# Kernel tuning notes

Hardware: AMD Instinct MI355X
Metric: run time of the kernel (lower is better)

The kernel has to match this reference:

```python
import jax, jax.numpy as jnp
import numpy as np

N_NODES = 100_000
N_EDGES = 1_600_000
IN_DIM = 500
HID = 128
OUT = 16
DEG = 3          # Chebyshev 'order' -> DEG+1 basis terms
N_KAN_USED = 2   # forward applies kan_layers[:num_layers-1] with num_layers=3


def spmm(edge_index, h):
    # torch.sparse.mm(A, h) with A = COO(edge_index, ones, (N, N)):
    # out[row] = sum over edges of h[col]
    return jax.ops.segment_sum(h[edge_index[1]], edge_index[0], num_segments=N_NODES)


def cheb_kan(h, coeffs):
    # ChebyKANLayer: t = tanh(h); basis T_k(t) = cos(k*arccos(t)) computed via
    # the (mathematically identical, numerically stable) recurrence.
    t = jnp.tanh(h)                                  # [N, HID]
    Ts = [jnp.ones_like(t), t]
    for _ in range(DEG - 1):
        Ts.append(2.0 * t * Ts[-1] - Ts[-2])
    basis = jnp.stack(Ts, axis=-1)                   # [N, HID, DEG+1]
    return jnp.einsum('nid,iod->no', basis, coeffs)  # [N, HID]


def setup_inputs() -> dict:
    key = jax.random.key(0)
    ks = jax.random.split(key, 6)
    x = jax.random.normal(ks[0], (N_NODES, IN_DIM), dtype=jnp.float32)
    edge_index = jax.random.randint(ks[1], (2, N_EDGES), 0, N_NODES)
    W_in = jax.random.normal(ks[2], (IN_DIM, HID), dtype=jnp.float32) / np.sqrt(IN_DIM)
    cheb_coeffs = jax.random.normal(ks[3], (N_KAN_USED, HID, HID, DEG + 1),
                                    dtype=jnp.float32) / (HID * (DEG + 1))
    W_out = jax.random.normal(ks[4], (HID, OUT), dtype=jnp.float32) / np.sqrt(HID)
    return {"x": x, "edge_index": edge_index, "W_in": W_in,
            "cheb_coeffs": cheb_coeffs, "W_out": W_out}


def reference(x, edge_index, W_in, cheb_coeffs, W_out):
    h = x @ W_in                      # linear_input (no bias)
    # dropout is identity at inference
    h = spmm(edge_index, h)           # sparse adjacency aggregation
    for l in range(N_KAN_USED):
        h = cheb_kan(h, cheb_coeffs[l])
        h = spmm(edge_index, h)
    logits = h @ W_out                # output_layer (no bias)
    return jax.nn.log_softmax(logits, axis=-1)
```

## Files before the change

kernel.cpp:

```cpp
#include <hip/hip_runtime.h>
#include <hip/hip_bf16.h>

#define N_NODES 100000
#define N_EDGES 1600000
#define IN_DIM  500
#define HID     128
#define KDIM    512
#define NB      782
#define BCAP    4096

typedef __attribute__((ext_vector_type(8))) short bf16x8;
typedef __attribute__((ext_vector_type(4))) float f32x4;

__device__ inline short f2bf(float x) {
    union { float f; unsigned u; } v; v.f = x;
    unsigned r = (v.u + 0x7FFFu + ((v.u >> 16) & 1u)) >> 16;
    return (short)r;
}
__device__ inline float bf_lo(unsigned u) { union { unsigned u; float f; } v; v.u = u << 16; return v.f; }
__device__ inline float bf_hi(unsigned u) { union { unsigned u; float f; } v; v.u = u & 0xFFFF0000u; return v.f; }
__device__ inline float bf2f(unsigned short s) { union { unsigned u; float f; } v; v.u = ((unsigned)s) << 16; return v.f; }


__global__ __launch_bounds__(256) void bin_kernel(const int* __restrict__ ei,
                                                  int* __restrict__ bcnt,
                                                  unsigned* __restrict__ buf) {
    int e = blockIdx.x * 256 + threadIdx.x;
    if (e < N_EDGES) {
        int r = ei[e];
        int c = ei[N_EDGES + e];
        int b = r >> 7;
        int p = atomicAdd(&bcnt[b * 16], 1);
        if (p < BCAP) buf[b * BCAP + p] = ((unsigned)(r & 127) << 17) | (unsigned)c;
    }
}

__global__ __launch_bounds__(1024) void bscan_kernel(const int* __restrict__ bcnt,
                                                     int* __restrict__ bbase) {
    __shared__ int buf[1024];
    const int tid = threadIdx.x;
    int v = (tid < NB) ? bcnt[tid * 16] : 0;
    buf[tid] = v;
    __syncthreads();
    for (int off = 1; off < 1024; off <<= 1) {
        int t = (tid >= off) ? buf[tid - off] : 0;
        __syncthreads();
        buf[tid] += t;
        __syncthreads();
    }
    if (tid < NB) bbase[tid] = buf[tid] - v;
}

__global__ __launch_bounds__(256) void place_kernel(const unsigned* __restrict__ buf,
                                                    const int* __restrict__ bcnt,
                                                    const int* __restrict__ bbase,
                                                    int* __restrict__ row_start,
                                                    int* __restrict__ col_sorted) {
    __shared__ int hist[128];
    __shared__ int scan[128];
    __shared__ int cur[128];
    const int b = blockIdx.x, tid = threadIdx.x;
    int cnt = bcnt[b * 16]; if (cnt > BCAP) cnt = BCAP;
    const int base = bbase[b];
    if (tid < 128) hist[tid] = 0;
    __syncthreads();
    for (int i = tid; i < cnt; i += 256)
        atomicAdd(&hist[buf[b * BCAP + i] >> 17], 1);
    __syncthreads();
    if (tid < 128) scan[tid] = hist[tid];
    __syncthreads();
    for (int off = 1; off < 128; off <<= 1) {
        int t = (tid < 128 && tid >= off) ? scan[tid - off] : 0;
        __syncthreads();
        if (tid < 128) scan[tid] += t;
        __syncthreads();
    }
    if (tid < 128) {
        int excl = scan[tid] - hist[tid] + base;
        cur[tid] = excl;
        int r = b * 128 + tid;
        if (r < N_NODES) row_start[r] = excl;
        if (r == N_NODES - 1) row_start[N_NODES] = excl + hist[tid];
    }
    __syncthreads();
    for (int i = tid; i < cnt; i += 256) {
        unsigned u = buf[b * BCAP + i];
        int rl = (int)(u >> 17);
        int c  = (int)(u & 0x1FFFFu);
        int pos = atomicAdd(&cur[rl], 1);
        col_sorted[pos] = c;
    }
}

__global__ __launch_bounds__(256) void repack_cheb(const float* __restrict__ cheb,
                                                   unsigned short* __restrict__ Bmat) {
    int idx = blockIdx.x * 256 + threadIdx.x;
    int l = idx >> 16;
    int rem = idx & 65535;
    int o = rem >> 9;
    int k = rem & 511;
    int i = k >> 2;
    int d = k & 3;
    Bmat[idx] = (unsigned short)f2bf(cheb[l * 65536 + i * 512 + o * 4 + d]);
}
__global__ __launch_bounds__(256) void repack_w(const float* __restrict__ W,
                                                unsigned short* __restrict__ Wmat) {
    int idx = blockIdx.x * 256 + threadIdx.x;
    int o = idx >> 9;
    int k = idx & 511;
    Wmat[idx] = (k < IN_DIM) ? (unsigned short)f2bf(W[k * HID + o]) : 0;
}

__global__ __launch_bounds__(256, 3) void gemm_xw(const float* __restrict__ x,
                                                  const unsigned short* __restrict__ Wmat,
                                                  unsigned short* __restrict__ out) {
    __shared__ __align__(16) short As[128][40];
    __shared__ __align__(16) short Bs[128][40];
    const int tid  = threadIdx.x;
    const int lane = tid & 63;
    const int wave = tid >> 6;
    const int quad = lane >> 4;
    const int l16  = lane & 15;
    const int n0   = blockIdx.x * 128;
    const int lr   = tid >> 1;
    const int lh   = tid & 1;

    f32x4 acc[2][8];
#pragma unroll
    for (int mt = 0; mt < 2; mt++)
#pragma unroll
        for (int nt = 0; nt < 8; nt++)
#pragma unroll
            for (int r = 0; r < 4; r++) acc[mt][nt][r] = 0.f;

    for (int kt = 0; kt < 16; kt++) {
        const int k0 = kt * 32;
        {
            int n = n0 + lr; if (n >= N_NODES) n = N_NODES - 1;
            const float* src = x + (long)n * IN_DIM + k0 + lh * 16;
            const int kb = k0 + lh * 16;
            float v[16];
            if (kb + 16 <= IN_DIM) {
                const float4* s4 = (const float4*)src;
                float4 a0 = s4[0], a1 = s4[1], a2 = s4[2], a3 = s4[3];
                v[0]=a0.x; v[1]=a0.y; v[2]=a0.z; v[3]=a0.w;
                v[4]=a1.x; v[5]=a1.y; v[6]=a1.z; v[7]=a1.w;
                v[8]=a2.x; v[9]=a2.y; v[10]=a2.z; v[11]=a2.w;
                v[12]=a3.x; v[13]=a3.y; v[14]=a3.z; v[15]=a3.w;
            } else {
#pragma unroll
                for (int q = 0; q < 16; q++) v[q] = (kb + q < IN_DIM) ? src[q] : 0.f;
            }
            short tmp[16];
#pragma unroll
            for (int q = 0; q < 16; q++) tmp[q] = f2bf(v[q]);
            *(bf16x8*)&As[lr][lh * 16]     = *(bf16x8*)&tmp[0];
            *(bf16x8*)&As[lr][lh * 16 + 8] = *(bf16x8*)&tmp[8];
        }
        for (int idx = tid; idx < 512; idx += 256) {
            int m = idx >> 2, kq = idx & 3;
            *(bf16x8*)&Bs[m][kq * 8] = *(const bf16x8*)&Wmat[m * 512 + k0 + kq * 8];
        }
        __syncthreads();
        bf16x8 a0 = *(const bf16x8*)&As[wave * 32 + l16][quad * 8];
        bf16x8 a1 = *(const bf16x8*)&As[wave * 32 + 16 + l16][quad * 8];
#pragma unroll
        for (int nt = 0; nt < 8; nt++) {
            bf16x8 b = *(const bf16x8*)&Bs[nt * 16 + l16][quad * 8];
            acc[0][nt] = __builtin_amdgcn_mfma_f32_16x16x32_bf16(a0, b, acc[0][nt], 0, 0, 0);
            acc[1][nt] = __builtin_amdgcn_mfma_f32_16x16x32_bf16(a1, b, acc[1][nt], 0, 0, 0);
        }
        __syncthreads();
    }
#pragma unroll
    for (int mt = 0; mt < 2; mt++) {
        int mrow = n0 + wave * 32 + mt * 16 + quad * 4;
#pragma unroll
        for (int r = 0; r < 4; r++) {
            int n = mrow + r;
            if (n < N_NODES) {
#pragma unroll
                for (int nt = 0; nt < 8; nt++)
                    out[(long)n * HID + nt * 16 + l16] = (unsigned short)f2bf(acc[mt][nt][r]);
            }
        }
    }
}

__global__ __launch_bounds__(256, 3) void cheb_gemm(const unsigned short* __restrict__ h,
                                                    const unsigned short* __restrict__ Bmat,
                                                    unsigned short* __restrict__ out) {
    __shared__ __align__(16) short As[128][40];
    __shared__ __align__(16) short Bs[128][40];
    const int tid  = threadIdx.x;
    const int lane = tid & 63;
    const int wave = tid >> 6;
    const int quad = lane >> 4;
    const int l16  = lane & 15;
    const int n0   = blockIdx.x * 128;
    const int lr   = tid >> 1;
    const int lh   = tid & 1;

    f32x4 acc[2][8];
#pragma unroll
    for (int mt = 0; mt < 2; mt++)
#pragma unroll
        for (int nt = 0; nt < 8; nt++)
#pragma unroll
            for (int r = 0; r < 4; r++) acc[mt][nt][r] = 0.f;

    for (int kt = 0; kt < 16; kt++) {
        const int k0 = kt * 32;
        const int i0 = kt * 8;
        {
            int n = n0 + lr; if (n >= N_NODES) n = N_NODES - 1;
            const ushort4 hv = *(const ushort4*)(h + (long)n * HID + i0 + lh * 4);
            float hx[4] = {bf2f(hv.x), bf2f(hv.y), bf2f(hv.z), bf2f(hv.w)};
            short tmp[16];
#pragma unroll
            for (int q = 0; q < 4; q++) {
                float xx = fminf(fmaxf(hx[q], -15.f), 15.f);
                float e  = __expf(2.f * xx);
                float t  = (e - 1.f) / (e + 1.f);
                float T2 = 2.f * t * t - 1.f;
                float T3 = 2.f * t * T2 - t;
                tmp[q * 4 + 0] = (short)0x3F80;
                tmp[q * 4 + 1] = f2bf(t);
                tmp[q * 4 + 2] = f2bf(T2);
                tmp[q * 4 + 3] = f2bf(T3);
            }
            *(bf16x8*)&As[lr][lh * 16]     = *(bf16x8*)&tmp[0];
            *(bf16x8*)&As[lr][lh * 16 + 8] = *(bf16x8*)&tmp[8];
        }
        for (int idx = tid; idx < 512; idx += 256) {
            int m = idx >> 2, kq = idx & 3;
            *(bf16x8*)&Bs[m][kq * 8] = *(const bf16x8*)&Bmat[m * 512 + k0 + kq * 8];
        }
        __syncthreads();
        bf16x8 a0 = *(const bf16x8*)&As[wave * 32 + l16][quad * 8];
        bf16x8 a1 = *(const bf16x8*)&As[wave * 32 + 16 + l16][quad * 8];
#pragma unroll
        for (int nt = 0; nt < 8; nt++) {
            bf16x8 b = *(const bf16x8*)&Bs[nt * 16 + l16][quad * 8];
            acc[0][nt] = __builtin_amdgcn_mfma_f32_16x16x32_bf16(a0, b, acc[0][nt], 0, 0, 0);
            acc[1][nt] = __builtin_amdgcn_mfma_f32_16x16x32_bf16(a1, b, acc[1][nt], 0, 0, 0);
        }
        __syncthreads();
    }
#pragma unroll
    for (int mt = 0; mt < 2; mt++) {
        int mrow = n0 + wave * 32 + mt * 16 + quad * 4;
#pragma unroll
        for (int r = 0; r < 4; r++) {
            int n = mrow + r;
            if (n < N_NODES) {
#pragma unroll
                for (int nt = 0; nt < 8; nt++)
                    out[(long)n * HID + nt * 16 + l16] = (unsigned short)f2bf(acc[mt][nt][r]);
            }
        }
    }
}

__global__ __launch_bounds__(256) void spmm_gather(const int* __restrict__ row_start,
                                                   const int* __restrict__ col_sorted,
                                                   const unsigned short* __restrict__ h,
                                                   unsigned short* __restrict__ out) {
    const int wid  = (blockIdx.x * 256 + threadIdx.x) >> 6;
    const int lane = threadIdx.x & 63;
    if (wid >= N_NODES) return;
    const int s = row_start[wid];
    const int e = row_start[wid + 1];
    const unsigned* __restrict__ h1 = (const unsigned*)h;
    float ax0 = 0.f, ay0 = 0.f, ax1 = 0.f, ay1 = 0.f;
    float ax2 = 0.f, ay2 = 0.f, ax3 = 0.f, ay3 = 0.f;
    int j = s;
    for (; j + 3 < e; j += 4) {
        int c0 = col_sorted[j];
        int c1 = col_sorted[j + 1];
        int c2 = col_sorted[j + 2];
        int c3 = col_sorted[j + 3];
        unsigned u0 = h1[c0 * 64 + lane];
        unsigned u1 = h1[c1 * 64 + lane];
        unsigned u2 = h1[c2 * 64 + lane];
        unsigned u3 = h1[c3 * 64 + lane];
        ax0 += bf_lo(u0); ay0 += bf_hi(u0);
        ax1 += bf_lo(u1); ay1 += bf_hi(u1);
        ax2 += bf_lo(u2); ay2 += bf_hi(u2);
        ax3 += bf_lo(u3); ay3 += bf_hi(u3);
    }
    for (; j < e; j++) {
        unsigned u = h1[col_sorted[j] * 64 + lane];
        ax0 += bf_lo(u); ay0 += bf_hi(u);
    }
    ax0 += ax1 + ax2 + ax3; ay0 += ay1 + ay2 + ay3;
    unsigned lo = (unsigned)(unsigned short)f2bf(ax0);
    unsigned hi = (unsigned)(unsigned short)f2bf(ay0);
    ((unsigned*)out)[wid * 64 + lane] = lo | (hi << 16);
}

__global__ __launch_bounds__(256) void out_kernel(const unsigned short* __restrict__ h,
                                                  const float* __restrict__ Wo,
                                                  float* __restrict__ out) {
    __shared__ float Ws[HID * 16];
    __shared__ float Hs[16][HID];
    const int tid = threadIdx.x;
    const int n0 = blockIdx.x * 16;
    for (int idx = tid; idx < HID * 16; idx += 256) Ws[idx] = Wo[idx];
    const unsigned* h1 = (const unsigned*)h;
    for (int idx = tid; idx < 16 * 64; idx += 256) {
        int nl = idx >> 6;
        int kp = idx & 63;
        unsigned u = h1[(n0 + nl) * 64 + kp];
        Hs[nl][kp * 2]     = bf_lo(u);
        Hs[nl][kp * 2 + 1] = bf_hi(u);
    }
    __syncthreads();
    const int nl = tid >> 4;
    const int o  = tid & 15;
    float acc = 0.f;
#pragma unroll
    for (int k = 0; k < HID; k++) acc += Hs[nl][k] * Ws[k * 16 + o];
    float mx = acc;
#pragma unroll
    for (int m = 8; m >= 1; m >>= 1) mx = fmaxf(mx, __shfl_xor(mx, m));
    float ex = expf(acc - mx);
    float se = ex;
#pragma unroll
    for (int m = 8; m >= 1; m >>= 1) se += __shfl_xor(se, m);
    out[(n0 + nl) * 16 + o] = acc - mx - logf(se);
}


extern "C" void kernel_launch(void* const* d_in, const int* in_sizes, int n_in,
                              void* d_out, int out_size, void* d_ws, size_t ws_size,
                              hipStream_t stream) {
    const float* x     = (const float*)d_in[0];
    const int*   ei    = (const int*)d_in[1];
    const float* W_in  = (const float*)d_in[2];
    const float* cheb  = (const float*)d_in[3];
    const float* W_out = (const float*)d_in[4];
    float* out = (float*)d_out;

    char* p = (char*)d_ws;
    unsigned short* hA   = (unsigned short*)p; p += (size_t)N_NODES * HID * 2;
    unsigned short* hB   = (unsigned short*)p; p += (size_t)N_NODES * HID * 2;
    int*   col_sorted    = (int*)p;            p += (size_t)N_EDGES * 4;
    unsigned short* Bmat = (unsigned short*)p; p += (size_t)2 * HID * KDIM * 2;
    unsigned short* Wmat = (unsigned short*)p; p += (size_t)HID * KDIM * 2;
    int*   row_start     = (int*)p;            p += (size_t)(N_NODES + 1) * 4;
    int*   bcnt          = (int*)p;            p += (size_t)NB * 16 * 4;
    int*   bbase         = (int*)p;            p += (size_t)NB * 4;

    unsigned* bbuf = (unsigned*)hA;

    const int nblk_gemm = (N_NODES + 127) / 128;
    const int nblk_edge = N_EDGES / 256;
    const int nblk_spmm = (N_NODES + 3) / 4;
    const int nblk_out  = N_NODES / 16;

    hipMemsetAsync(bcnt, 0, (size_t)NB * 16 * 4, stream);
    bin_kernel<<<nblk_edge, 256, 0, stream>>>(ei, bcnt, bbuf);
    bscan_kernel<<<1, 1024, 0, stream>>>(bcnt, bbase);
    place_kernel<<<NB, 256, 0, stream>>>(bbuf, bcnt, bbase, row_start, col_sorted);
    repack_cheb<<<2 * HID * KDIM / 256, 256, 0, stream>>>(cheb, Bmat);
    repack_w<<<HID * KDIM / 256, 256, 0, stream>>>(W_in, Wmat);

    gemm_xw<<<nblk_gemm, 256, 0, stream>>>(x, Wmat, hA);
    spmm_gather<<<nblk_spmm, 256, 0, stream>>>(row_start, col_sorted, hA, hB);

    cheb_gemm<<<nblk_gemm, 256, 0, stream>>>(hB, Bmat, hA);
    spmm_gather<<<nblk_spmm, 256, 0, stream>>>(row_start, col_sorted, hA, hB);

    cheb_gemm<<<nblk_gemm, 256, 0, stream>>>(hB, Bmat + HID * KDIM, hA);
    spmm_gather<<<nblk_spmm, 256, 0, stream>>>(row_start, col_sorted, hA, hB);

    out_kernel<<<nblk_out, 256, 0, stream>>>(hB, W_out, out);
}
```

Baseline: 740.9 us.

## Load GEMM operands directly into MFMA registers, dropping LDS staging and barriers

Both the input projection GEMM and the Chebyshev GEMM stop staging A and B tiles through shared memory. Each lane now loads its MFMA fragment straight from global memory (x rows, h rows, and the weight matrix through cache) and computes the tanh/Chebyshev basis per lane. This removes the LDS round trips and the two __syncthreads per k-step, and the k-loop is unrolled by two. In exchange, every wave re-reads the weight fragments from L1/L2, the x loads become 32-byte strided accesses per lane, and launch bounds are relaxed to allow more registers per thread.

```diff
diff --git a/kernel.cpp b/kernel.cpp
--- a/kernel.cpp
+++ b/kernel.cpp
@@ -111,19 +111,20 @@
     Wmat[idx] = (k < IN_DIM) ? (unsigned short)f2bf(W[k * HID + o]) : 0;
 }
 
-__global__ __launch_bounds__(256, 3) void gemm_xw(const float* __restrict__ x,
+__global__ __launch_bounds__(256, 2) void gemm_xw(const float* __restrict__ x,
                                                   const unsigned short* __restrict__ Wmat,
                                                   unsigned short* __restrict__ out) {
-    __shared__ __align__(16) short As[128][40];
-    __shared__ __align__(16) short Bs[128][40];
     const int tid  = threadIdx.x;
     const int lane = tid & 63;
     const int wave = tid >> 6;
     const int quad = lane >> 4;
     const int l16  = lane & 15;
     const int n0   = blockIdx.x * 128;
-    const int lr   = tid >> 1;
-    const int lh   = tid & 1;
+
+    int row0 = n0 + wave * 32 + l16;      if (row0 >= N_NODES) row0 = N_NODES - 1;
+    int row1 = n0 + wave * 32 + 16 + l16; if (row1 >= N_NODES) row1 = N_NODES - 1;
+    const float* __restrict__ xr0 = x + (long)row0 * IN_DIM + quad * 8;
+    const float* __restrict__ xr1 = x + (long)row1 * IN_DIM + quad * 8;
 
     f32x4 acc[2][8];
 #pragma unroll
@@ -133,44 +134,43 @@
 #pragma unroll
             for (int r = 0; r < 4; r++) acc[mt][nt][r] = 0.f;
 
-    for (int kt = 0; kt < 16; kt++) {
+#pragma unroll 2
+    for (int kt = 0; kt < 15; kt++) {
         const int k0 = kt * 32;
-        {
-            int n = n0 + lr; if (n >= N_NODES) n = N_NODES - 1;
-            const float* src = x + (long)n * IN_DIM + k0 + lh * 16;
-            const int kb = k0 + lh * 16;
-            float v[16];
-            if (kb + 16 <= IN_DIM) {
-                const float4* s4 = (const float4*)src;
-                float4 a0 = s4[0], a1 = s4[1], a2 = s4[2], a3 = s4[3];
-                v[0]=a0.x; v[1]=a0.y; v[2]=a0.z; v[3]=a0.w;
-                v[4]=a1.x; v[5]=a1.y; v[6]=a1.z; v[7]=a1.w;
-                v[8]=a2.x; v[9]=a2.y; v[10]=a2.z; v[11]=a2.w;
-                v[12]=a3.x; v[13]=a3.y; v[14]=a3.z; v[15]=a3.w;
-            } else {
-#pragma unroll
-                for (int q = 0; q < 16; q++) v[q] = (kb + q < IN_DIM) ? src[q] : 0.f;
-            }
-            short tmp[16];
-#pragma unroll
-            for (int q = 0; q < 16; q++) tmp[q] = f2bf(v[q]);
-            *(bf16x8*)&As[lr][lh * 16]     = *(bf16x8*)&tmp[0];
-            *(bf16x8*)&As[lr][lh * 16 + 8] = *(bf16x8*)&tmp[8];
-        }
-        for (int idx = tid; idx < 512; idx += 256) {
-            int m = idx >> 2, kq = idx & 3;
-            *(bf16x8*)&Bs[m][kq * 8] = *(const bf16x8*)&Wmat[m * 512 + k0 + kq * 8];
-        }
-        __syncthreads();
-        bf16x8 a0 = *(const bf16x8*)&As[wave * 32 + l16][quad * 8];
-        bf16x8 a1 = *(const bf16x8*)&As[wave * 32 + 16 + l16][quad * 8];
+        float4 f0a = *(const float4*)(xr0 + k0);
+        float4 f0b = *(const float4*)(xr0 + k0 + 4);
+        float4 f1a = *(const float4*)(xr1 + k0);
+        float4 f1b = *(const float4*)(xr1 + k0 + 4);
+        short t0[8] = {f2bf(f0a.x), f2bf(f0a.y), f2bf(f0a.z), f2bf(f0a.w),
+                       f2bf(f0b.x), f2bf(f0b.y), f2bf(f0b.z), f2bf(f0b.w)};
+        short t1[8] = {f2bf(f1a.x), f2bf(f1a.y), f2bf(f1a.z), f2bf(f1a.w),
+                       f2bf(f1b.x), f2bf(f1b.y), f2bf(f1b.z), f2bf(f1b.w)};
+        bf16x8 a0 = *(bf16x8*)t0;
+        bf16x8 a1 = *(bf16x8*)t1;
 #pragma unroll
         for (int nt = 0; nt < 8; nt++) {
-            bf16x8 b = *(const bf16x8*)&Bs[nt * 16 + l16][quad * 8];
+            bf16x8 b = *(const bf16x8*)&Wmat[(nt * 16 + l16) * 512 + k0 + quad * 8];
             acc[0][nt] = __builtin_amdgcn_mfma_f32_16x16x32_bf16(a0, b, acc[0][nt], 0, 0, 0);
             acc[1][nt] = __builtin_amdgcn_mfma_f32_16x16x32_bf16(a1, b, acc[1][nt], 0, 0, 0);
         }
-        __syncthreads();
+    }
+    {
+        const int k0 = 480;
+        short t0[8], t1[8];
+#pragma unroll
+        for (int q = 0; q < 8; q++) {
+            int kk = k0 + quad * 8 + q;
+            t0[q] = (kk < IN_DIM) ? f2bf(xr0[k0 + q]) : (short)0;
+            t1[q] = (kk < IN_DIM) ? f2bf(xr1[k0 + q]) : (short)0;
+        }
+        bf16x8 a0 = *(bf16x8*)t0;
+        bf16x8 a1 = *(bf16x8*)t1;
+#pragma unroll
+        for (int nt = 0; nt < 8; nt++) {
+            bf16x8 b = *(const bf16x8*)&Wmat[(nt * 16 + l16) * 512 + k0 + quad * 8];
+            acc[0][nt] = __builtin_amdgcn_mfma_f32_16x16x32_bf16(a0, b, acc[0][nt], 0, 0, 0);
+            acc[1][nt] = __builtin_amdgcn_mfma_f32_16x16x32_bf16(a1, b, acc[1][nt], 0, 0, 0);
+        }
     }
 #pragma unroll
     for (int mt = 0; mt < 2; mt++) {
@@ -187,19 +187,20 @@
     }
 }
 
-__global__ __launch_bounds__(256, 3) void cheb_gemm(const unsigned short* __restrict__ h,
+__global__ __launch_bounds__(256, 2) void cheb_gemm(const unsigned short* __restrict__ h,
                                                     const unsigned short* __restrict__ Bmat,
                                                     unsigned short* __restrict__ out) {
-    __shared__ __align__(16) short As[128][40];
-    __shared__ __align__(16) short Bs[128][40];
     const int tid  = threadIdx.x;
     const int lane = tid & 63;
     const int wave = tid >> 6;
     const int quad = lane >> 4;
     const int l16  = lane & 15;
     const int n0   = blockIdx.x * 128;
-    const int lr   = tid >> 1;
-    const int lh   = tid & 1;
+
+    int row0 = n0 + wave * 32 + l16;      if (row0 >= N_NODES) row0 = N_NODES - 1;
+    int row1 = n0 + wave * 32 + 16 + l16; if (row1 >= N_NODES) row1 = N_NODES - 1;
+    const unsigned* __restrict__ hr0 = (const unsigned*)(h + (long)row0 * HID) + quad;
+    const unsigned* __restrict__ hr1 = (const unsigned*)(h + (long)row1 * HID) + quad;
 
     f32x4 acc[2][8];
 #pragma unroll
@@ -209,43 +210,50 @@
 #pragma unroll
             for (int r = 0; r < 4; r++) acc[mt][nt][r] = 0.f;
 
+#pragma unroll 2
     for (int kt = 0; kt < 16; kt++) {
         const int k0 = kt * 32;
-        const int i0 = kt * 8;
+        unsigned u0 = hr0[kt * 4];
+        unsigned u1 = hr1[kt * 4];
+        short t0[8], t1[8];
         {
-            int n = n0 + lr; if (n >= N_NODES) n = N_NODES - 1;
-            const ushort4 hv = *(const ushort4*)(h + (long)n * HID + i0 + lh * 4);
-            float hx[4] = {bf2f(hv.x), bf2f(hv.y), bf2f(hv.z), bf2f(hv.w)};
-            short tmp[16];
-#pragma unroll
-            for (int q = 0; q < 4; q++) {
+            float hx[2] = {bf_lo(u0), bf_hi(u0)};
+#pragma unroll
+            for (int q = 0; q < 2; q++) {
                 float xx = fminf(fmaxf(hx[q], -15.f), 15.f);
                 float e  = __expf(2.f * xx);
                 float t  = (e - 1.f) / (e + 1.f);
                 float T2 = 2.f * t * t - 1.f;
                 float T3 = 2.f * t * T2 - t;
-                tmp[q * 4 + 0] = (short)0x3F80;
-                tmp[q * 4 + 1] = f2bf(t);
-                tmp[q * 4 + 2] = f2bf(T2);
-                tmp[q * 4 + 3] = f2bf(T3);
+                t0[q * 4 + 0] = (short)0x3F80;
+                t0[q * 4 + 1] = f2bf(t);
+                t0[q * 4 + 2] = f2bf(T2);
+                t0[q * 4 + 3] = f2bf(T3);
             }
-            *(bf16x8*)&As[lr][lh * 16]     = *(bf16x8*)&tmp[0];
-            *(bf16x8*)&As[lr][lh * 16 + 8] = *(bf16x8*)&tmp[8];
-        }
-        for (int idx = tid; idx < 512; idx += 256) {
-            int m = idx >> 2, kq = idx & 3;
-            *(bf16x8*)&Bs[m][kq * 8] = *(const bf16x8*)&Bmat[m * 512 + k0 + kq * 8];
-        }
-        __syncthreads();
-        bf16x8 a0 = *(const bf16x8*)&As[wave * 32 + l16][quad * 8];
-        bf16x8 a1 = *(const bf16x8*)&As[wave * 32 + 16 + l16][quad * 8];
+        }
+        {
+            float hx[2] = {bf_lo(u1), bf_hi(u1)};
+#pragma unroll
+            for (int q = 0; q < 2; q++) {
+                float xx = fminf(fmaxf(hx[q], -15.f), 15.f);
+                float e  = __expf(2.f * xx);
+                float t  = (e - 1.f) / (e + 1.f);
+                float T2 = 2.f * t * t - 1.f;
+                float T3 = 2.f * t * T2 - t;
+                t1[q * 4 + 0] = (short)0x3F80;
+                t1[q * 4 + 1] = f2bf(t);
+                t1[q * 4 + 2] = f2bf(T2);
+                t1[q * 4 + 3] = f2bf(T3);
+            }
+        }
+        bf16x8 a0 = *(bf16x8*)t0;
+        bf16x8 a1 = *(bf16x8*)t1;
 #pragma unroll
         for (int nt = 0; nt < 8; nt++) {
-            bf16x8 b = *(const bf16x8*)&Bs[nt * 16 + l16][quad * 8];
+            bf16x8 b = *(const bf16x8*)&Bmat[(nt * 16 + l16) * 512 + k0 + quad * 8];
             acc[0][nt] = __builtin_amdgcn_mfma_f32_16x16x32_bf16(a0, b, acc[0][nt], 0, 0, 0);
             acc[1][nt] = __builtin_amdgcn_mfma_f32_16x16x32_bf16(a1, b, acc[1][nt], 0, 0, 0);
         }
-        __syncthreads();
     }
 #pragma unroll
     for (int mt = 0; mt < 2; mt++) {
```

After: 883.2 us. 1.19x slower.

## Double-buffer LDS tiles and prefetch next k-tile in dense GEMM kernels

Applied to the files above, without the earlier changes.

Both gemm_xw and cheb_gemm now use two shared-memory buffers and register-prefetch the next k-slice of A and B while MFMAs run on the current one. This cuts the barriers per k-step from two to one and hides global load latency behind compute. In exchange it doubles LDS use and raises register pressure from the prefetch registers, which could lower occupancy under the launch_bounds(256,3) hint.

```diff
diff --git a/kernel.cpp b/kernel.cpp
--- a/kernel.cpp
+++ b/kernel.cpp
@@ -114,8 +114,8 @@
 __global__ __launch_bounds__(256, 3) void gemm_xw(const float* __restrict__ x,
                                                   const unsigned short* __restrict__ Wmat,
                                                   unsigned short* __restrict__ out) {
-    __shared__ __align__(16) short As[128][40];
-    __shared__ __align__(16) short Bs[128][40];
+    __shared__ __align__(16) short As[2][128][40];
+    __shared__ __align__(16) short Bs[2][128][40];
     const int tid  = threadIdx.x;
     const int lane = tid & 63;
     const int wave = tid >> 6;
@@ -124,6 +124,11 @@
     const int n0   = blockIdx.x * 128;
     const int lr   = tid >> 1;
     const int lh   = tid & 1;
+    const int bm   = tid >> 2;
+    const int bkq  = tid & 3;
+
+    int nA = n0 + lr; if (nA >= N_NODES) nA = N_NODES - 1;
+    const float* __restrict__ xrow = x + (long)nA * IN_DIM;
 
     f32x4 acc[2][8];
 #pragma unroll
@@ -133,45 +138,60 @@
 #pragma unroll
             for (int r = 0; r < 4; r++) acc[mt][nt][r] = 0.f;
 
-    for (int kt = 0; kt < 16; kt++) {
-        const int k0 = kt * 32;
-        {
-            int n = n0 + lr; if (n >= N_NODES) n = N_NODES - 1;
-            const float* src = x + (long)n * IN_DIM + k0 + lh * 16;
-            const int kb = k0 + lh * 16;
-            float v[16];
-            if (kb + 16 <= IN_DIM) {
-                const float4* s4 = (const float4*)src;
-                float4 a0 = s4[0], a1 = s4[1], a2 = s4[2], a3 = s4[3];
-                v[0]=a0.x; v[1]=a0.y; v[2]=a0.z; v[3]=a0.w;
-                v[4]=a1.x; v[5]=a1.y; v[6]=a1.z; v[7]=a1.w;
-                v[8]=a2.x; v[9]=a2.y; v[10]=a2.z; v[11]=a2.w;
-                v[12]=a3.x; v[13]=a3.y; v[14]=a3.z; v[15]=a3.w;
-            } else {
-#pragma unroll
-                for (int q = 0; q < 16; q++) v[q] = (kb + q < IN_DIM) ? src[q] : 0.f;
-            }
-            short tmp[16];
-#pragma unroll
-            for (int q = 0; q < 16; q++) tmp[q] = f2bf(v[q]);
-            *(bf16x8*)&As[lr][lh * 16]     = *(bf16x8*)&tmp[0];
-            *(bf16x8*)&As[lr][lh * 16 + 8] = *(bf16x8*)&tmp[8];
-        }
-        for (int idx = tid; idx < 512; idx += 256) {
-            int m = idx >> 2, kq = idx & 3;
-            *(bf16x8*)&Bs[m][kq * 8] = *(const bf16x8*)&Wmat[m * 512 + k0 + kq * 8];
-        }
-        __syncthreads();
-        bf16x8 a0 = *(const bf16x8*)&As[wave * 32 + l16][quad * 8];
-        bf16x8 a1 = *(const bf16x8*)&As[wave * 32 + 16 + l16][quad * 8];
+    auto loadA = [&](int kt, float (&v)[16]) {
+        const int kb = kt * 32 + lh * 16;
+        if (kb + 16 <= IN_DIM) {
+            const float4* s4 = (const float4*)(xrow + kb);
+            float4 a0 = s4[0], a1 = s4[1], a2 = s4[2], a3 = s4[3];
+            v[0]=a0.x; v[1]=a0.y; v[2]=a0.z; v[3]=a0.w;
+            v[4]=a1.x; v[5]=a1.y; v[6]=a1.z; v[7]=a1.w;
+            v[8]=a2.x; v[9]=a2.y; v[10]=a2.z; v[11]=a2.w;
+            v[12]=a3.x; v[13]=a3.y; v[14]=a3.z; v[15]=a3.w;
+        } else {
+#pragma unroll
+            for (int q = 0; q < 16; q++) v[q] = (kb + q < IN_DIM) ? xrow[kb + q] : 0.f;
+        }
+    };
+    auto loadB = [&](int kt, bf16x8 (&w)[2]) {
+        w[0] = *(const bf16x8*)&Wmat[bm * 512 + kt * 32 + bkq * 8];
+        w[1] = *(const bf16x8*)&Wmat[(bm + 64) * 512 + kt * 32 + bkq * 8];
+    };
+    auto storeA = [&](int buf, const float (&v)[16]) {
+        short t[16];
+#pragma unroll
+        for (int q = 0; q < 16; q++) t[q] = f2bf(v[q]);
+        *(bf16x8*)&As[buf][lr][lh * 16]     = *(bf16x8*)&t[0];
+        *(bf16x8*)&As[buf][lr][lh * 16 + 8] = *(bf16x8*)&t[8];
+    };
+    auto storeB = [&](int buf, const bf16x8 (&w)[2]) {
+        *(bf16x8*)&Bs[buf][bm][bkq * 8]      = w[0];
+        *(bf16x8*)&Bs[buf][bm + 64][bkq * 8] = w[1];
+    };
+    auto mfmaTile = [&](int buf) {
+        bf16x8 a0 = *(const bf16x8*)&As[buf][wave * 32 + l16][quad * 8];
+        bf16x8 a1 = *(const bf16x8*)&As[buf][wave * 32 + 16 + l16][quad * 8];
 #pragma unroll
         for (int nt = 0; nt < 8; nt++) {
-            bf16x8 b = *(const bf16x8*)&Bs[nt * 16 + l16][quad * 8];
+            bf16x8 b = *(const bf16x8*)&Bs[buf][nt * 16 + l16][quad * 8];
             acc[0][nt] = __builtin_amdgcn_mfma_f32_16x16x32_bf16(a0, b, acc[0][nt], 0, 0, 0);
             acc[1][nt] = __builtin_amdgcn_mfma_f32_16x16x32_bf16(a1, b, acc[1][nt], 0, 0, 0);
         }
-        __syncthreads();
-    }
+    };
+
+    float  va[16], vb[16];
+    bf16x8 wa[2],  wb[2];
+    loadA(0, va); loadB(0, wa);
+    for (int kt = 0; kt < 16; kt += 2) {
+        storeA(0, va); storeB(0, wa);
+        loadA(kt + 1, vb); loadB(kt + 1, wb);
+        __syncthreads();
+        mfmaTile(0);
+        storeA(1, vb); storeB(1, wb);
+        if (kt + 2 < 16) { loadA(kt + 2, va); loadB(kt + 2, wa); }
+        __syncthreads();
+        mfmaTile(1);
+    }
+
 #pragma unroll
     for (int mt = 0; mt < 2; mt++) {
         int mrow = n0 + wave * 32 + mt * 16 + quad * 4;
@@ -190,8 +210,8 @@
 __global__ __launch_bounds__(256, 3) void cheb_gemm(const unsigned short* __restrict__ h,
                                                     const unsigned short* __restrict__ Bmat,
                                                     unsigned short* __restrict__ out) {
-    __shared__ __align__(16) short As[128][40];
-    __shared__ __align__(16) short Bs[128][40];
+    __shared__ __align__(16) short As[2][128][40];
+    __shared__ __align__(16) short Bs[2][128][40];
     const int tid  = threadIdx.x;
     const int lane = tid & 63;
     const int wave = tid >> 6;
@@ -200,6 +220,11 @@
     const int n0   = blockIdx.x * 128;
     const int lr   = tid >> 1;
     const int lh   = tid & 1;
+    const int bm   = tid >> 2;
+    const int bkq  = tid & 3;
+
+    int nA = n0 + lr; if (nA >= N_NODES) nA = N_NODES - 1;
+    const unsigned short* __restrict__ hrow = h + (long)nA * HID;
 
     f32x4 acc[2][8];
 #pragma unroll
@@ -209,44 +234,60 @@
 #pragma unroll
             for (int r = 0; r < 4; r++) acc[mt][nt][r] = 0.f;
 
-    for (int kt = 0; kt < 16; kt++) {
-        const int k0 = kt * 32;
-        const int i0 = kt * 8;
-        {
-            int n = n0 + lr; if (n >= N_NODES) n = N_NODES - 1;
-            const ushort4 hv = *(const ushort4*)(h + (long)n * HID + i0 + lh * 4);
-            float hx[4] = {bf2f(hv.x), bf2f(hv.y), bf2f(hv.z), bf2f(hv.w)};
-            short tmp[16];
-#pragma unroll
-            for (int q = 0; q < 4; q++) {
-                float xx = fminf(fmaxf(hx[q], -15.f), 15.f);
-                float e  = __expf(2.f * xx);
-                float t  = (e - 1.f) / (e + 1.f);
-                float T2 = 2.f * t * t - 1.f;
-                float T3 = 2.f * t * T2 - t;
-                tmp[q * 4 + 0] = (short)0x3F80;
-                tmp[q * 4 + 1] = f2bf(t);
-                tmp[q * 4 + 2] = f2bf(T2);
-                tmp[q * 4 + 3] = f2bf(T3);
-            }
-            *(bf16x8*)&As[lr][lh * 16]     = *(bf16x8*)&tmp[0];
-            *(bf16x8*)&As[lr][lh * 16 + 8] = *(bf16x8*)&tmp[8];
-        }
-        for (int idx = tid; idx < 512; idx += 256) {
-            int m = idx >> 2, kq = idx & 3;
-            *(bf16x8*)&Bs[m][kq * 8] = *(const bf16x8*)&Bmat[m * 512 + k0 + kq * 8];
-        }
-        __syncthreads();
-        bf16x8 a0 = *(const bf16x8*)&As[wave * 32 + l16][quad * 8];
-        bf16x8 a1 = *(const bf16x8*)&As[wave * 32 + 16 + l16][quad * 8];
+    auto loadA = [&](int kt, ushort4& v) {
+        v = *(const ushort4*)(hrow + kt * 8 + lh * 4);
+    };
+    auto loadB = [&](int kt, bf16x8 (&w)[2]) {
+        w[0] = *(const bf16x8*)&Bmat[bm * 512 + kt * 32 + bkq * 8];
+        w[1] = *(const bf16x8*)&Bmat[(bm + 64) * 512 + kt * 32 + bkq * 8];
+    };
+    auto storeA = [&](int buf, const ushort4& v) {
+        float hx[4] = {bf2f(v.x), bf2f(v.y), bf2f(v.z), bf2f(v.w)};
+        short t[16];
+#pragma unroll
+        for (int q = 0; q < 4; q++) {
+            float xx = fminf(fmaxf(hx[q], -15.f), 15.f);
+            float e  = __expf(2.f * xx);
+            float tt = (e - 1.f) / (e + 1.f);
+            float T2 = 2.f * tt * tt - 1.f;
+            float T3 = 2.f * tt * T2 - tt;
+            t[q * 4 + 0] = (short)0x3F80;
+            t[q * 4 + 1] = f2bf(tt);
+            t[q * 4 + 2] = f2bf(T2);
+            t[q * 4 + 3] = f2bf(T3);
+        }
+        *(bf16x8*)&As[buf][lr][lh * 16]     = *(bf16x8*)&t[0];
+        *(bf16x8*)&As[buf][lr][lh * 16 + 8] = *(bf16x8*)&t[8];
+    };
+    auto storeB = [&](int buf, const bf16x8 (&w)[2]) {
+        *(bf16x8*)&Bs[buf][bm][bkq * 8]      = w[0];
+        *(bf16x8*)&Bs[buf][bm + 64][bkq * 8] = w[1];
+    };
+    auto mfmaTile = [&](int buf) {
+        bf16x8 a0 = *(const bf16x8*)&As[buf][wave * 32 + l16][quad * 8];
+        bf16x8 a1 = *(const bf16x8*)&As[buf][wave * 32 + 16 + l16][quad * 8];
 #pragma unroll
         for (int nt = 0; nt < 8; nt++) {
-            bf16x8 b = *(const bf16x8*)&Bs[nt * 16 + l16][quad * 8];
+            bf16x8 b = *(const bf16x8*)&Bs[buf][nt * 16 + l16][quad * 8];
             acc[0][nt] = __builtin_amdgcn_mfma_f32_16x16x32_bf16(a0, b, acc[0][nt], 0, 0, 0);
             acc[1][nt] = __builtin_amdgcn_mfma_f32_16x16x32_bf16(a1, b, acc[1][nt], 0, 0, 0);
         }
-        __syncthreads();
-    }
+    };
+
+    ushort4 va, vb;
+    bf16x8  wa[2], wb[2];
+    loadA(0, va); loadB(0, wa);
+    for (int kt = 0; kt < 16; kt += 2) {
+        storeA(0, va); storeB(0, wa);
+        loadA(kt + 1, vb); loadB(kt + 1, wb);
+        __syncthreads();
+        mfmaTile(0);
+        storeA(1, vb); storeB(1, wb);
+        if (kt + 2 < 16) { loadA(kt + 2, va); loadB(kt + 2, wa); }
+        __syncthreads();
+        mfmaTile(1);
+    }
+
 #pragma unroll
     for (int mt = 0; mt < 2; mt++) {
         int mrow = n0 + wave * 32 + mt * 16 + quad * 4;
```

After: 721.8 us. -2.6%, faster.
